# Kernel optimization log

Hardware: AMD Instinct MI355X
Metric: run time of the kernel (lower is better)

## Reference

```python
import jax, jax.numpy as jnp
import numpy as np


def setup_inputs() -> dict:
    key = jax.random.key(0)
    k1, k2, k3 = jax.random.split(key, 3)
    B, D, F = 4096, 1024, 16384  # batch, input_dim, dict_size
    x = jax.random.normal(k1, (B, D), dtype=jnp.float32)
    W_enc = jax.random.normal(k2, (F, D), dtype=jnp.float32) * (1.0 / np.sqrt(D))
    b_enc = jnp.zeros((F,), dtype=jnp.float32)
    W_dec = jax.random.normal(k3, (D, F), dtype=jnp.float32)
    # decoder columns are unit-normalized (as in _normalize_decoder)
    W_dec = W_dec / jnp.clip(jnp.linalg.norm(W_dec, axis=0, keepdims=True), 1e-8)
    b_dec = jnp.zeros((D,), dtype=jnp.float32)
    return {"x": x, "W_enc": W_enc, "b_enc": b_enc, "W_dec": W_dec, "b_dec": b_dec, "k": 32}


def reference(x, W_enc, b_enc, W_dec, b_dec, k):
    # encode: z_pre = (x - b_dec) @ W_enc^T + b_enc   -> [B, F]
    x_centered = x - b_dec
    z_pre = jnp.einsum('bd,fd->bf', x_centered, W_enc) + b_enc
    # activate: TopK(ReLU(z_pre)) via top_k + relu + scatter
    topk_vals, topk_idx = jax.lax.top_k(z_pre, k)           # [B, k]
    B = z_pre.shape[0]
    rows = jnp.arange(B)[:, None]                            # [B, 1]
    z = jnp.zeros_like(z_pre).at[rows, topk_idx].set(jax.nn.relu(topk_vals))
    # decode: x_hat = z @ W_dec^T + b_dec (dense matmul over sparse z)
    x_hat = jnp.einsum('bf,df->bd', z, W_dec) + b_dec
    return (x_hat, z, z_pre)
```

## Files before the change

kernel.cpp:

```cpp
#include <hip/hip_runtime.h>
#include <cstdint>
#include <cfloat>
#include <cstddef>

#define MAXK 128

typedef __attribute__((ext_vector_type(8))) short bf16x8;
typedef __attribute__((ext_vector_type(4))) float f32x4;

__device__ __forceinline__ void split8(const float4& v0, const float4& v1,
                                       uint4& hp, uint4& lp)
{
    float vv[8] = {v0.x, v0.y, v0.z, v0.w, v1.x, v1.y, v1.z, v1.w};
    unsigned h[8], l[8];
    #pragma unroll
    for (int i = 0; i < 8; ++i) {
        unsigned u  = __float_as_uint(vv[i]);
        unsigned hb = u & 0xFFFF0000u;
        float lf    = vv[i] - __uint_as_float(hb);
        h[i] = u;
        l[i] = __float_as_uint(lf);
    }
    hp.x = (h[0] >> 16) | (h[1] & 0xFFFF0000u);
    hp.y = (h[2] >> 16) | (h[3] & 0xFFFF0000u);
    hp.z = (h[4] >> 16) | (h[5] & 0xFFFF0000u);
    hp.w = (h[6] >> 16) | (h[7] & 0xFFFF0000u);
    lp.x = (l[0] >> 16) | (l[1] & 0xFFFF0000u);
    lp.y = (l[2] >> 16) | (l[3] & 0xFFFF0000u);
    lp.z = (l[4] >> 16) | (l[5] & 0xFFFF0000u);
    lp.w = (l[6] >> 16) | (l[7] & 0xFFFF0000u);
}

__device__ __forceinline__ void gload_lds16(const void* g, void* l)
{
    __builtin_amdgcn_global_load_lds(
        (const __attribute__((address_space(1))) unsigned int*)g,
        (__attribute__((address_space(3))) unsigned int*)l,
        16, 0, 0);
}

__global__ __launch_bounds__(256)
void prep_x_kernel(const float* __restrict__ x, const float* __restrict__ b_dec,
                   ushort* __restrict__ AhiP, ushort* __restrict__ AloP, int D)
{
    const int c   = blockIdx.x * 256 + threadIdx.x;
    const int t   = c >> 9;
    const int wc  = c & 511;
    const int rl  = wc >> 2;
    const int pkc = wc & 3;
    const int kc  = (pkc - (rl >> 1)) & 3;
    const int nkb = D >> 5;
    const int band = t / nkb, kblk = t - band * nkb;
    const int row = band * 128 + rl;
    const int k0  = kblk * 32 + kc * 8;

    const float* src = x + (size_t)row * D + k0;
    float4 v0 = *(const float4*)(src);
    float4 v1 = *(const float4*)(src + 4);
    const float* bd = b_dec + k0;
    float4 d0 = *(const float4*)(bd);
    float4 d1 = *(const float4*)(bd + 4);
    v0.x -= d0.x; v0.y -= d0.y; v0.z -= d0.z; v0.w -= d0.w;
    v1.x -= d1.x; v1.y -= d1.y; v1.z -= d1.z; v1.w -= d1.w;
    uint4 hp, lp;
    split8(v0, v1, hp, lp);
    const size_t off = (size_t)t * 4096 + (size_t)wc * 8;
    *(uint4*)&AhiP[off] = hp;
    *(uint4*)&AloP[off] = lp;
}

__global__ __launch_bounds__(256)
void prep_w_kernel(const float* __restrict__ Wenc,
                   ushort* __restrict__ WhiP, ushort* __restrict__ WloP, int D)
{
    const int c   = blockIdx.x * 256 + threadIdx.x;
    const int t   = c >> 10;
    const int wc  = c & 1023;
    const int rl  = wc >> 2;
    const int pkc = wc & 3;
    const int kc  = (pkc - (rl >> 1)) & 3;
    const int nkb = D >> 5;
    const int fband = t / nkb, kblk = t - fband * nkb;
    const int f   = fband * 256 + rl;
    const int k0  = kblk * 32 + kc * 8;

    const float* src = Wenc + (size_t)f * D + k0;
    float4 v0 = *(const float4*)(src);
    float4 v1 = *(const float4*)(src + 4);
    uint4 hp, lp;
    split8(v0, v1, hp, lp);
    const size_t off = (size_t)t * 8192 + (size_t)wc * 8;
    *(uint4*)&WhiP[off] = hp;
    *(uint4*)&WloP[off] = lp;
}

__global__ __launch_bounds__(256, 2)
void encode_gemm_pre(const ushort* __restrict__ AhiP, const ushort* __restrict__ AloP,
                     const ushort* __restrict__ WhiP, const ushort* __restrict__ WloP,
                     const float* __restrict__ b_enc, float* __restrict__ z_pre,
                     int D, int F)
{
    __shared__ ushort AsHi[4096];
    __shared__ ushort AsLo[4096];
    __shared__ ushort BsHi[8192];
    __shared__ ushort BsLo[8192];

    const int tid = threadIdx.x;
    const int bm  = blockIdx.y * 128;
    const int bn  = blockIdx.x * 256;

    const int lane = tid & 63;
    const int w    = tid >> 6;
    const int wm   = (w >> 1) * 64;
    const int wn   = (w & 1) * 128;
    const int fr   = lane & 15;
    const int q    = lane >> 4;
    const int nkb  = D >> 5;

    int aoff[4], boff[8];
    #pragma unroll
    for (int mi = 0; mi < 4; ++mi) {
        const int r = wm + mi * 16 + fr;
        aoff[mi] = r * 32 + (((q + (r >> 1)) & 3) * 8);
    }
    #pragma unroll
    for (int ni = 0; ni < 8; ++ni) {
        const int r = wn + ni * 16 + fr;
        boff[ni] = r * 32 + (((q + (r >> 1)) & 3) * 8);
    }

    f32x4 acc[4][8];
    #pragma unroll
    for (int mi = 0; mi < 4; ++mi)
        #pragma unroll
        for (int ni = 0; ni < 8; ++ni)
            acc[mi][ni] = (f32x4){0.f, 0.f, 0.f, 0.f};

    const char* aHi = (const char*)AhiP + (size_t)blockIdx.y * nkb * 8192;
    const char* aLo = (const char*)AloP + (size_t)blockIdx.y * nkb * 8192;
    const char* bHi = (const char*)WhiP + (size_t)blockIdx.x * nkb * 16384;
    const char* bLo = (const char*)WloP + (size_t)blockIdx.x * nkb * 16384;
    const int la16 = lane * 16;

    for (int kb = 0; kb < nkb; ++kb) {
        const char* pa = aHi + (size_t)kb * 8192;
        const char* pl = aLo + (size_t)kb * 8192;
        const char* pb = bHi + (size_t)kb * 16384;
        const char* pm = bLo + (size_t)kb * 16384;

        #pragma unroll
        for (int c = 0; c < 2; ++c) {
            const int off = (w * 2 + c) * 1024;
            gload_lds16(pa + off + la16, (char*)AsHi + off);
            gload_lds16(pl + off + la16, (char*)AsLo + off);
        }
        #pragma unroll
        for (int c = 0; c < 4; ++c) {
            const int off = (w * 4 + c) * 1024;
            gload_lds16(pb + off + la16, (char*)BsHi + off);
            gload_lds16(pm + off + la16, (char*)BsLo + off);
        }
        asm volatile("s_waitcnt vmcnt(0)" ::: "memory");
        __syncthreads();

        bf16x8 ahi[4], alo[4];
        #pragma unroll
        for (int mi = 0; mi < 4; ++mi) {
            ahi[mi] = *(const bf16x8*)&AsHi[aoff[mi]];
            alo[mi] = *(const bf16x8*)&AsLo[aoff[mi]];
        }
        #pragma unroll
        for (int ni = 0; ni < 8; ++ni) {
            bf16x8 bhi = *(const bf16x8*)&BsHi[boff[ni]];
            bf16x8 blo = *(const bf16x8*)&BsLo[boff[ni]];
            #pragma unroll
            for (int mi = 0; mi < 4; ++mi) {
                acc[mi][ni] = __builtin_amdgcn_mfma_f32_16x16x32_bf16(alo[mi], bhi, acc[mi][ni], 0, 0, 0);
                acc[mi][ni] = __builtin_amdgcn_mfma_f32_16x16x32_bf16(ahi[mi], blo, acc[mi][ni], 0, 0, 0);
                acc[mi][ni] = __builtin_amdgcn_mfma_f32_16x16x32_bf16(ahi[mi], bhi, acc[mi][ni], 0, 0, 0);
            }
        }
        __syncthreads();
    }

    #pragma unroll
    for (int ni = 0; ni < 8; ++ni) {
        const int col = bn + wn + ni * 16 + fr;
        const float be = b_enc[col];
        #pragma unroll
        for (int mi = 0; mi < 4; ++mi) {
            const int rbase = bm + wm + mi * 16 + q * 4;
            float* dst = z_pre + (size_t)rbase * F + col;
            #pragma unroll
            for (int r = 0; r < 4; ++r)
                dst[(size_t)r * F] = acc[mi][ni][r] + be;
        }
    }
}

__global__ __launch_bounds__(256, 2)
void encode_gemm_bf16x3(const float* __restrict__ x, const float* __restrict__ Wenc,
                        const float* __restrict__ b_enc, const float* __restrict__ b_dec,
                        float* __restrict__ z_pre, int D, int F)
{
    constexpr int BM = 128, BN = 256, BK = 32;
    __shared__ ushort AsHi[BM * BK];
    __shared__ ushort AsLo[BM * BK];
    __shared__ ushort BsHi[BN * BK];
    __shared__ ushort BsLo[BN * BK];

    const int tid = threadIdx.x;
    const int bm  = blockIdx.y * BM;
    const int bn  = blockIdx.x * BN;

    const int lane = tid & 63;
    const int w    = tid >> 6;
    const int wm   = (w >> 1) * 64;
    const int wn   = (w & 1) * 128;
    const int fr   = lane & 15;
    const int q    = lane >> 4;

    int aoff[4], boff[8];
    #pragma unroll
    for (int mi = 0; mi < 4; ++mi) {
        const int r = wm + mi * 16 + fr;
        aoff[mi] = r * 32 + (((q + (r >> 1)) & 3) * 8);
    }
    #pragma unroll
    for (int ni = 0; ni < 8; ++ni) {
        const int r = wn + ni * 16 + fr;
        boff[ni] = r * 32 + (((q + (r >> 1)) & 3) * 8);
    }

    f32x4 acc[4][8];
    #pragma unroll
    for (int mi = 0; mi < 4; ++mi)
        #pragma unroll
        for (int ni = 0; ni < 8; ++ni)
            acc[mi][ni] = (f32x4){0.f, 0.f, 0.f, 0.f};

    for (int k0 = 0; k0 < D; k0 += BK) {
        #pragma unroll
        for (int j = 0; j < 2; ++j) {
            const int task = tid + 256 * j;
            const int row = task >> 2, kc = task & 3;
            const float* src = x + (size_t)(bm + row) * D + k0 + kc * 8;
            float4 v0 = *(const float4*)(src);
            float4 v1 = *(const float4*)(src + 4);
            const float* bd = b_dec + k0 + kc * 8;
            float4 d0 = *(const float4*)(bd);
            float4 d1 = *(const float4*)(bd + 4);
            v0.x -= d0.x; v0.y -= d0.y; v0.z -= d0.z; v0.w -= d0.w;
            v1.x -= d1.x; v1.y -= d1.y; v1.z -= d1.z; v1.w -= d1.w;
            uint4 hp, lp;
            split8(v0, v1, hp, lp);
            const int off = row * 32 + (((kc + (row >> 1)) & 3) * 8);
            *(uint4*)&AsHi[off] = hp;
            *(uint4*)&AsLo[off] = lp;
        }
        #pragma unroll
        for (int j = 0; j < 4; ++j) {
            const int task = tid + 256 * j;
            const int row = task >> 2, kc = task & 3;
            const float* src = Wenc + (size_t)(bn + row) * D + k0 + kc * 8;
            float4 v0 = *(const float4*)(src);
            float4 v1 = *(const float4*)(src + 4);
            uint4 hp, lp;
            split8(v0, v1, hp, lp);
            const int off = row * 32 + (((kc + (row >> 1)) & 3) * 8);
            *(uint4*)&BsHi[off] = hp;
            *(uint4*)&BsLo[off] = lp;
        }
        __syncthreads();

        bf16x8 ahi[4], alo[4];
        #pragma unroll
        for (int mi = 0; mi < 4; ++mi) {
            ahi[mi] = *(const bf16x8*)&AsHi[aoff[mi]];
            alo[mi] = *(const bf16x8*)&AsLo[aoff[mi]];
        }
        #pragma unroll
        for (int ni = 0; ni < 8; ++ni) {
            bf16x8 bhi = *(const bf16x8*)&BsHi[boff[ni]];
            bf16x8 blo = *(const bf16x8*)&BsLo[boff[ni]];
            #pragma unroll
            for (int mi = 0; mi < 4; ++mi) {
                acc[mi][ni] = __builtin_amdgcn_mfma_f32_16x16x32_bf16(alo[mi], bhi, acc[mi][ni], 0, 0, 0);
                acc[mi][ni] = __builtin_amdgcn_mfma_f32_16x16x32_bf16(ahi[mi], blo, acc[mi][ni], 0, 0, 0);
                acc[mi][ni] = __builtin_amdgcn_mfma_f32_16x16x32_bf16(ahi[mi], bhi, acc[mi][ni], 0, 0, 0);
            }
        }
        __syncthreads();
    }

    #pragma unroll
    for (int ni = 0; ni < 8; ++ni) {
        const int col = bn + wn + ni * 16 + fr;
        const float be = b_enc[col];
        #pragma unroll
        for (int mi = 0; mi < 4; ++mi) {
            const int rbase = bm + wm + mi * 16 + q * 4;
            float* dst = z_pre + (size_t)rbase * F + col;
            #pragma unroll
            for (int r = 0; r < 4; ++r)
                dst[(size_t)r * F] = acc[mi][ni][r] + be;
        }
    }
}

__device__ __forceinline__ unsigned fkey(float f)
{
    unsigned u = __float_as_uint(f);
    return u ^ ((unsigned)((int)u >> 31) | 0x80000000u);
}
__device__ __forceinline__ float finv(unsigned k)
{
    unsigned u = (k & 0x80000000u) ? (k ^ 0x80000000u) : ~k;
    return __uint_as_float(u);
}

template <int NVEC>
__global__ __launch_bounds__(256)
void topk_kernel(const float* __restrict__ z_pre, float* __restrict__ z,
                 float* __restrict__ ws_vals, int* __restrict__ ws_idx,
                 const int* __restrict__ k_ptr,
                 const float* __restrict__ x, const float* __restrict__ Wenc,
                 const float* __restrict__ b_enc, const float* __restrict__ b_dec,
                 int F, int D)
{
    const int row = blockIdx.x;
    const int t   = threadIdx.x;
    const int k   = *k_ptr;
    const int nv4 = F >> 2;

    const float4* src = (const float4*)(z_pre + (size_t)row * F);
    float4 vals[NVEC];
    #pragma unroll
    for (int i = 0; i < NVEC; ++i) {
        const int p = t + 256 * i;
        if (p < nv4) vals[i] = src[p];
        else         vals[i] = make_float4(-FLT_MAX, -FLT_MAX, -FLT_MAX, -FLT_MAX);
    }

    __shared__ int hist[256];
    __shared__ int suffix[256];
    __shared__ int s_bin;
    __shared__ int c_hi_s, n_c_s, out_cnt;
    __shared__ int cand_idx[128];
    __shared__ float cand_val[128];
    __shared__ unsigned char cand_sel[128];

    unsigned prefix = 0;
    int rem = k;

    for (int pass = 0; pass < 4; ++pass) {
        const int shift = 24 - 8 * pass;
        hist[t] = 0;
        __syncthreads();
        #pragma unroll
        for (int i = 0; i < NVEC; ++i) {
            const float* vv = (const float*)&vals[i];
            #pragma unroll
            for (int j = 0; j < 4; ++j) {
                const unsigned key = fkey(vv[j]);
                const bool inb = (pass == 0) || ((key >> (shift + 8)) == prefix);
                if (inb) atomicAdd(&hist[(key >> shift) & 255], 1);
            }
        }
        __syncthreads();
        suffix[t] = hist[t];
        __syncthreads();
        #pragma unroll
        for (int off = 1; off < 256; off <<= 1) {
            const int add = (t + off < 256) ? suffix[t + off] : 0;
            __syncthreads();
            suffix[t] += add;
            __syncthreads();
        }
        const int sfx = suffix[t];
        const int nxt = (t < 255) ? suffix[t + 1] : 0;
        if (sfx >= rem && nxt < rem) s_bin = t;
        __syncthreads();
        const int b = s_bin;
        const int above = (b < 255) ? suffix[b + 1] : 0;
        rem -= above;
        prefix = (prefix << 8) | (unsigned)b;
        __syncthreads();
    }

    const float vT = finv(prefix);
    const float dlt = 1e-3f;
    const float hiThr = vT + dlt;
    const float loThr = vT - dlt;

    if (t == 0) { c_hi_s = 0; n_c_s = 0; out_cnt = 0; }
    __syncthreads();

    #pragma unroll
    for (int i = 0; i < NVEC; ++i) {
        const float* vv = (const float*)&vals[i];
        #pragma unroll
        for (int j = 0; j < 4; ++j) {
            const float v = vv[j];
            if (v > hiThr) {
                atomicAdd(&c_hi_s, 1);
            } else if (v > loThr) {
                const int s = atomicAdd(&n_c_s, 1);
                if (s < 128) { cand_idx[s] = (t + 256 * i) * 4 + j; cand_sel[s] = 0; }
            }
        }
    }
    __syncthreads();

    const int n_c = min(n_c_s, 128);

    {
        const int wv_id = t >> 6, ln = t & 63;
        const float* xr = x + (size_t)row * D;
        for (int c = wv_id; c < n_c; c += 4) {
            const int f = cand_idx[c];
            const float* wr = Wenc + (size_t)f * D;
            float s = 0.f;
            for (int d = ln * 4; d < D; d += 256) {
                float4 xv = *(const float4*)(xr + d);
                float4 bd = *(const float4*)(b_dec + d);
                float4 wv4 = *(const float4*)(wr + d);
                s = fmaf(xv.x - bd.x, wv4.x, s);
                s = fmaf(xv.y - bd.y, wv4.y, s);
                s = fmaf(xv.z - bd.z, wv4.z, s);
                s = fmaf(xv.w - bd.w, wv4.w, s);
            }
            #pragma unroll
            for (int o = 32; o > 0; o >>= 1) s += __shfl_down(s, o, 64);
            if (ln == 0) cand_val[c] = s + b_enc[f];
        }
    }
    __syncthreads();

    if (t == 0) {
        int need = k - c_hi_s;
        if (need > n_c) need = n_c;
        for (int it = 0; it < need; ++it) {
            int bi = -1; float bv = 0.f;
            for (int c = 0; c < n_c; ++c) {
                if (cand_sel[c]) continue;
                const float v = cand_val[c];
                if (bi < 0 || v > bv || (v == bv && cand_idx[c] < cand_idx[bi])) {
                    bi = c; bv = v;
                }
            }
            if (bi < 0) break;
            cand_sel[bi] = 1;
        }
    }
    __syncthreads();

    float4* dstz = (float4*)(z + (size_t)row * F);
    float*  wv   = ws_vals + (size_t)row * MAXK;
    int*    wi   = ws_idx  + (size_t)row * MAXK;

    #pragma unroll
    for (int i = 0; i < NVEC; ++i) {
        const int p4 = t + 256 * i;
        if (p4 < nv4) {
            const float* vv = (const float*)&vals[i];
            float4 outv;
            float* ov = (float*)&outv;
            #pragma unroll
            for (int j = 0; j < 4; ++j) {
                const int pos = p4 * 4 + j;
                const float v = vv[j];
                float zv = 0.f;
                bool sel = false;
                if (v > hiThr) {
                    zv = fmaxf(v, 0.f); sel = true;
                } else if (v > loThr) {
                    for (int c = 0; c < n_c; ++c) {
                        if (cand_idx[c] == pos) {
                            if (cand_sel[c]) { zv = fmaxf(cand_val[c], 0.f); sel = true; }
                            break;
                        }
                    }
                }
                ov[j] = zv;
                if (sel) {
                    const int s = atomicAdd(&out_cnt, 1);
                    if (s < MAXK) { wv[s] = zv; wi[s] = pos; }
                }
            }
            dstz[p4] = outv;
        }
    }
}

__global__ __launch_bounds__(256)
void transpose_kernel(const float* __restrict__ in, float* __restrict__ out,
                      int R, int C)
{
    __shared__ float tile[32][33];
    const int c0 = blockIdx.x * 32;
    const int r0 = blockIdx.y * 32;
    const int tx = threadIdx.x & 31;
    const int ty = threadIdx.x >> 5;

    #pragma unroll
    for (int i = ty; i < 32; i += 8) {
        const int r = r0 + i, c = c0 + tx;
        tile[i][tx] = (r < R && c < C) ? in[(size_t)r * C + c] : 0.f;
    }
    __syncthreads();
    #pragma unroll
    for (int i = ty; i < 32; i += 8) {
        const int c = c0 + i, r = r0 + tx;
        if (c < C && r < R) out[(size_t)c * R + r] = tile[tx][i];
    }
}

__global__ __launch_bounds__(256)
void decode_kernel(const float* __restrict__ WdT, const float* __restrict__ wvals,
                   const int* __restrict__ widx, const float* __restrict__ b_dec,
                   float* __restrict__ x_hat, const int* __restrict__ k_ptr, int D)
{
    const int row = blockIdx.x;
    const int t   = threadIdx.x;
    int k = *k_ptr;
    if (k > MAXK) k = MAXK;

    const float* wv = wvals + (size_t)row * MAXK;
    const int*   wi = widx  + (size_t)row * MAXK;

    for (int d0 = t * 4; d0 < D; d0 += 1024) {
        float4 acc = *(const float4*)(b_dec + d0);
        for (int j = 0; j < k; ++j) {
            const float v = wv[j];
            const int   f = wi[j];
            const float4 w = *(const float4*)(WdT + (size_t)f * D + d0);
            acc.x = fmaf(v, w.x, acc.x);
            acc.y = fmaf(v, w.y, acc.y);
            acc.z = fmaf(v, w.z, acc.z);
            acc.w = fmaf(v, w.w, acc.w);
        }
        *(float4*)(x_hat + (size_t)row * D + d0) = acc;
    }
}

extern "C" void kernel_launch(void* const* d_in, const int* in_sizes, int n_in,
                              void* d_out, int out_size, void* d_ws, size_t ws_size,
                              hipStream_t stream)
{
    const float* x     = (const float*)d_in[0];
    const float* W_enc = (const float*)d_in[1];
    const float* b_enc = (const float*)d_in[2];
    const float* W_dec = (const float*)d_in[3];
    const float* b_dec = (const float*)d_in[4];
    const int*   k_ptr = (const int*)d_in[5];

    const int F = in_sizes[2];
    const int D = in_sizes[4];
    const int B = in_sizes[0] / D;

    float* x_hat = (float*)d_out;
    float* z     = x_hat + (size_t)B * D;
    float* z_pre = z + (size_t)B * F;

    float* WdT = (float*)d_ws;
    float* wv  = WdT + (size_t)F * D;
    int*   wi  = (int*)(wv + (size_t)B * MAXK);
    char*  extra = (char*)(wi + (size_t)B * MAXK);

    const size_t base_need  = (size_t)F * D * 4 + (size_t)B * MAXK * 8;
    const size_t extra_need = (size_t)B * D * 4 + (size_t)F * D * 4;
    const bool use_pre = (ws_size >= base_need + extra_need) &&
                         (D % 32 == 0) && (B % 128 == 0) && (F % 256 == 0);

    if (use_pre) {
        ushort* AhiP = (ushort*)extra;
        ushort* AloP = AhiP + (size_t)B * D;
        ushort* WhiP = AloP + (size_t)B * D;
        ushort* WloP = WhiP + (size_t)F * D;

        prep_x_kernel<<<(B * (D / 8)) / 256, 256, 0, stream>>>(x, b_dec, AhiP, AloP, D);
        prep_w_kernel<<<(F * (D / 8)) / 256, 256, 0, stream>>>(W_enc, WhiP, WloP, D);
        encode_gemm_pre<<<dim3(F / 256, B / 128), 256, 0, stream>>>(
            AhiP, AloP, WhiP, WloP, b_enc, z_pre, D, F);
    } else {
        encode_gemm_bf16x3<<<dim3(F / 256, B / 128), 256, 0, stream>>>(
            x, W_enc, b_enc, b_dec, z_pre, D, F);
    }

    transpose_kernel<<<dim3((F + 31) / 32, (D + 31) / 32), 256, 0, stream>>>(
        W_dec, WdT, D, F);

    const int nv4  = F / 4;
    const int nvec = (nv4 + 255) / 256;
    if (nvec <= 4)
        topk_kernel<4><<<B, 256, 0, stream>>>(z_pre, z, wv, wi, k_ptr, x, W_enc, b_enc, b_dec, F, D);
    else if (nvec <= 8)
        topk_kernel<8><<<B, 256, 0, stream>>>(z_pre, z, wv, wi, k_ptr, x, W_enc, b_enc, b_dec, F, D);
    else if (nvec <= 16)
        topk_kernel<16><<<B, 256, 0, stream>>>(z_pre, z, wv, wi, k_ptr, x, W_enc, b_enc, b_dec, F, D);
    else
        topk_kernel<32><<<B, 256, 0, stream>>>(z_pre, z, wv, wi, k_ptr, x, W_enc, b_enc, b_dec, F, D);

    decode_kernel<<<B, 256, 0, stream>>>(WdT, wv, wi, b_dec, x_hat, k_ptr, D);
}
```

Measured before the change: 1.285 ms.

## Shorten top-k radix select to two passes with per-wave histograms; stage decode indices

The top-k radix select now runs two 8-bit passes instead of four. It uses per-wavefront shared histograms to cut atomic contention and a shuffle-based suffix scan in place of the barrier-heavy shared-memory scan. The threshold becomes a key range, so the existing exact-rescore candidate window is widened to cover the remaining low 16 bits. The decode kernel stages the top-k values and indices in shared memory and unrolls by two with dual accumulators. The risk is that a coarser threshold pushes more than 128 near-threshold candidates into the overflow buffer, which could silently drop correct top-k entries.

```diff
diff --git a/kernel.cpp b/kernel.cpp
--- a/kernel.cpp
+++ b/kernel.cpp
@@ -332,6 +332,8 @@
     const int t   = threadIdx.x;
     const int k   = *k_ptr;
     const int nv4 = F >> 2;
+    const int wv_id = t >> 6;
+    const int ln    = t & 63;
 
     const float4* src = (const float4*)(z_pre + (size_t)row * F);
     float4 vals[NVEC];
@@ -342,9 +344,9 @@
         else         vals[i] = make_float4(-FLT_MAX, -FLT_MAX, -FLT_MAX, -FLT_MAX);
     }
 
-    __shared__ int hist[256];
-    __shared__ int suffix[256];
-    __shared__ int s_bin;
+    __shared__ int hist[4][256];
+    __shared__ int waveTot[4];
+    __shared__ int s_bin, s_above;
     __shared__ int c_hi_s, n_c_s, out_cnt;
     __shared__ int cand_idx[128];
     __shared__ float cand_val[128];
@@ -353,9 +355,10 @@
     unsigned prefix = 0;
     int rem = k;
 
-    for (int pass = 0; pass < 4; ++pass) {
+    #pragma unroll
+    for (int pass = 0; pass < 2; ++pass) {
         const int shift = 24 - 8 * pass;
-        hist[t] = 0;
+        hist[0][t] = 0; hist[1][t] = 0; hist[2][t] = 0; hist[3][t] = 0;
         __syncthreads();
         #pragma unroll
         for (int i = 0; i < NVEC; ++i) {
@@ -364,34 +367,37 @@
             for (int j = 0; j < 4; ++j) {
                 const unsigned key = fkey(vv[j]);
                 const bool inb = (pass == 0) || ((key >> (shift + 8)) == prefix);
-                if (inb) atomicAdd(&hist[(key >> shift) & 255], 1);
+                if (inb) atomicAdd(&hist[wv_id][(key >> shift) & 255], 1);
             }
         }
         __syncthreads();
-        suffix[t] = hist[t];
-        __syncthreads();
-        #pragma unroll
-        for (int off = 1; off < 256; off <<= 1) {
-            const int add = (t + off < 256) ? suffix[t + off] : 0;
-            __syncthreads();
-            suffix[t] += add;
-            __syncthreads();
-        }
-        const int sfx = suffix[t];
-        const int nxt = (t < 255) ? suffix[t + 1] : 0;
-        if (sfx >= rem && nxt < rem) s_bin = t;
-        __syncthreads();
-        const int b = s_bin;
-        const int above = (b < 255) ? suffix[b + 1] : 0;
-        rem -= above;
-        prefix = (prefix << 8) | (unsigned)b;
-        __syncthreads();
-    }
-
-    const float vT = finv(prefix);
+        const int cnt = hist[0][t] + hist[1][t] + hist[2][t] + hist[3][t];
+        int s = cnt;
+        #pragma unroll
+        for (int off = 1; off < 64; off <<= 1) {
+            const int tmp = __shfl_down(s, off, 64);
+            if (ln + off < 64) s += tmp;
+        }
+        if (ln == 0) waveTot[wv_id] = s;
+        __syncthreads();
+        int add = 0;
+        #pragma unroll
+        for (int w2 = 0; w2 < 4; ++w2)
+            if (w2 > wv_id) add += waveTot[w2];
+        const int sfx = s + add;
+        const int nxt = sfx - cnt;
+        if (sfx >= rem && nxt < rem) { s_bin = t; s_above = nxt; }
+        __syncthreads();
+        rem -= s_above;
+        prefix = (prefix << 8) | (unsigned)s_bin;
+        __syncthreads();
+    }
+
+    const unsigned keyLo = prefix << 16;
+    const unsigned keyHi = keyLo | 0xFFFFu;
     const float dlt = 1e-3f;
-    const float hiThr = vT + dlt;
-    const float loThr = vT - dlt;
+    const float hiThr = finv(keyHi) + dlt;
+    const float loThr = finv(keyLo) - dlt;
 
     if (t == 0) { c_hi_s = 0; n_c_s = 0; out_cnt = 0; }
     __syncthreads();
@@ -415,7 +421,6 @@
     const int n_c = min(n_c_s, 128);
 
     {
-        const int wv_id = t >> 6, ln = t & 63;
         const float* xr = x + (size_t)row * D;
         for (int c = wv_id; c < n_c; c += 4) {
             const int f = cand_idx[c];
@@ -521,26 +526,47 @@
                    const int* __restrict__ widx, const float* __restrict__ b_dec,
                    float* __restrict__ x_hat, const int* __restrict__ k_ptr, int D)
 {
+    __shared__ float sv[MAXK];
+    __shared__ int   si[MAXK];
     const int row = blockIdx.x;
     const int t   = threadIdx.x;
     int k = *k_ptr;
     if (k > MAXK) k = MAXK;
 
-    const float* wv = wvals + (size_t)row * MAXK;
-    const int*   wi = widx  + (size_t)row * MAXK;
+    if (t < MAXK) {
+        sv[t] = wvals[(size_t)row * MAXK + t];
+        si[t] = widx [(size_t)row * MAXK + t];
+    }
+    __syncthreads();
 
     for (int d0 = t * 4; d0 < D; d0 += 1024) {
-        float4 acc = *(const float4*)(b_dec + d0);
-        for (int j = 0; j < k; ++j) {
-            const float v = wv[j];
-            const int   f = wi[j];
-            const float4 w = *(const float4*)(WdT + (size_t)f * D + d0);
-            acc.x = fmaf(v, w.x, acc.x);
-            acc.y = fmaf(v, w.y, acc.y);
-            acc.z = fmaf(v, w.z, acc.z);
-            acc.w = fmaf(v, w.w, acc.w);
-        }
-        *(float4*)(x_hat + (size_t)row * D + d0) = acc;
+        float4 acc0 = *(const float4*)(b_dec + d0);
+        float4 acc1 = make_float4(0.f, 0.f, 0.f, 0.f);
+        int j = 0;
+        for (; j + 2 <= k; j += 2) {
+            const float v0 = sv[j],     v1 = sv[j + 1];
+            const int   f0 = si[j],     f1 = si[j + 1];
+            const float4 w0 = *(const float4*)(WdT + (size_t)f0 * D + d0);
+            const float4 w1 = *(const float4*)(WdT + (size_t)f1 * D + d0);
+            acc0.x = fmaf(v0, w0.x, acc0.x);
+            acc0.y = fmaf(v0, w0.y, acc0.y);
+            acc0.z = fmaf(v0, w0.z, acc0.z);
+            acc0.w = fmaf(v0, w0.w, acc0.w);
+            acc1.x = fmaf(v1, w1.x, acc1.x);
+            acc1.y = fmaf(v1, w1.y, acc1.y);
+            acc1.z = fmaf(v1, w1.z, acc1.z);
+            acc1.w = fmaf(v1, w1.w, acc1.w);
+        }
+        if (j < k) {
+            const float v0 = sv[j];
+            const float4 w0 = *(const float4*)(WdT + (size_t)si[j] * D + d0);
+            acc0.x = fmaf(v0, w0.x, acc0.x);
+            acc0.y = fmaf(v0, w0.y, acc0.y);
+            acc0.z = fmaf(v0, w0.z, acc0.z);
+            acc0.w = fmaf(v0, w0.w, acc0.w);
+        }
+        acc0.x += acc1.x; acc0.y += acc1.y; acc0.z += acc1.z; acc0.w += acc1.w;
+        *(float4*)(x_hat + (size_t)row * D + d0) = acc0;
     }
 }
 
```

New measurement: 1.229 ms. 1.05x faster.
